# Performance work log

Measured on AMD Instinct MI355X. Metric: run time of the kernel, lower is better.

The kernel has to match this reference:

```python
import jax, jax.numpy as jnp
import numpy as np

EMBED_DIM = 1024
NUM_HEADS = 16
HEAD_DIM = EMBED_DIM // NUM_HEADS
EPS = 1e-5


def setup_inputs() -> dict:
    key = jax.random.key(0)
    ks = jax.random.split(key, 14)
    B, S, E = 2, 2048, EMBED_DIM
    s = 1.0 / np.sqrt(E)
    inp = {
        "x": jax.random.normal(ks[0], (B, S, E), dtype=jnp.float32),
        "Wq": jax.random.normal(ks[1], (E, E), dtype=jnp.float32) * s,
        "bq": jax.random.normal(ks[2], (E,), dtype=jnp.float32) * 0.01,
        "Wk": jax.random.normal(ks[3], (E, E), dtype=jnp.float32) * s,
        "bk": jax.random.normal(ks[4], (E,), dtype=jnp.float32) * 0.01,
        "Wv": jax.random.normal(ks[5], (E, E), dtype=jnp.float32) * s,
        "bv": jax.random.normal(ks[6], (E,), dtype=jnp.float32) * 0.01,
        "Wo": jax.random.normal(ks[7], (E, E), dtype=jnp.float32) * s,
        "bo": jax.random.normal(ks[8], (E,), dtype=jnp.float32) * 0.01,
        "qn_w": jnp.ones((HEAD_DIM,), jnp.float32) + 0.1 * jax.random.normal(ks[9], (HEAD_DIM,), jnp.float32),
        "qn_b": 0.1 * jax.random.normal(ks[10], (HEAD_DIM,), jnp.float32),
        "kn_w": jnp.ones((HEAD_DIM,), jnp.float32) + 0.1 * jax.random.normal(ks[11], (HEAD_DIM,), jnp.float32),
        "kn_b": 0.1 * jax.random.normal(ks[12], (HEAD_DIM,), jnp.float32),
    }
    return inp


def _layernorm(t, w, b):
    # normalize over last axis (head_dim), matching eqx.nn.LayerNorm(eps=1e-5)
    mu = jnp.mean(t, axis=-1, keepdims=True)
    var = jnp.mean(jnp.square(t - mu), axis=-1, keepdims=True)
    return (t - mu) * jax.lax.rsqrt(var + EPS) * w + b


def reference(x, Wq, bq, Wk, bk, Wv, bv, Wo, bo, qn_w, qn_b, kn_w, kn_b):
    B, S, E = x.shape
    H, D = NUM_HEADS, HEAD_DIM
    q = (x @ Wq.T + bq).reshape(B, S, H, D)
    k = (x @ Wk.T + bk).reshape(B, S, H, D)
    v = (x @ Wv.T + bv).reshape(B, S, H, D)
    q = _layernorm(q, qn_w, qn_b)
    k = _layernorm(k, kn_w, kn_b)
    scale = D ** (-0.5)
    # [B,H,S,S] score matrix (faithful to naive implementation)
    scores = jnp.einsum("bqhd,bkhd->bhqk", q, k) * scale
    attn = jax.nn.softmax(scores, axis=-1)
    out = jnp.einsum("bhqk,bkhd->bqhd", attn, v).reshape(B, S, E)
    return out @ Wo.T + bo
```

## Files before the change

kernel.cpp:

```cpp
#include <hip/hip_runtime.h>
#include <stdint.h>


typedef __bf16 bf16_t;
typedef __bf16 bf16x8 __attribute__((ext_vector_type(8)));
typedef __bf16 bf16x4 __attribute__((ext_vector_type(4)));
typedef __bf16 bf16x2 __attribute__((ext_vector_type(2)));
typedef float f32x4 __attribute__((ext_vector_type(4)));
typedef float f32x16 __attribute__((ext_vector_type(16)));
typedef uint32_t u32x4 __attribute__((ext_vector_type(4)));

#define S_LEN 2048
#define QSCALE 0.1803368801f

__device__ __forceinline__ void load_lds16(const void* g, void* l) {
  __builtin_amdgcn_global_load_lds((__attribute__((address_space(1))) void*)g,
                                   (__attribute__((address_space(3))) void*)l,
                                   16, 0, 0);
}

__device__ __forceinline__ f32x4 mfma16(bf16x8 a, bf16x8 b, f32x4 c) {
  return __builtin_amdgcn_mfma_f32_16x16x32_bf16(a, b, c, 0, 0, 0);
}

__device__ __forceinline__ f32x16 mfma32(bf16x8 a, bf16x8 b, f32x16 c) {
  return __builtin_amdgcn_mfma_f32_32x32x16_bf16(a, b, c, 0, 0, 0);
}

__device__ __forceinline__ uint32_t pk_bf16(float a, float b) {
  bf16x2 v; v[0] = (bf16_t)a; v[1] = (bf16_t)b;
  return __builtin_bit_cast(uint32_t, v);
}

__device__ __forceinline__ void plswap(uint32_t& a, uint32_t& b) {
  asm volatile("v_permlane32_swap_b32 %0, %1" : "+v"(a), "+v"(b));
}

__global__ void cvt_all(const float* __restrict__ x, const float* __restrict__ Wq,
                        const float* __restrict__ Wk, const float* __restrict__ Wv,
                        const float* __restrict__ Wo,
                        bf16_t* __restrict__ xb, bf16_t* __restrict__ Wb,
                        bf16_t* __restrict__ Wob) {
  const int bid = blockIdx.x;
  const float* src; bf16_t* dst; int idx;
  if (bid < 4096) { src = x; dst = xb; idx = bid; }
  else {
    const int r = bid - 4096, rg = r >> 10;
    idx = r & 1023;
    if (rg == 0)      { src = Wq; dst = Wb; }
    else if (rg == 1) { src = Wk; dst = Wb + (1 << 20); }
    else if (rg == 2) { src = Wv; dst = Wb + (2 << 20); }
    else              { src = Wo; dst = Wob; }
  }
  const int i = (idx * 256 + threadIdx.x) * 4;
  float4 v = *reinterpret_cast<const float4*>(src + i);
  bf16x4 o;
  o[0] = (bf16_t)v.x; o[1] = (bf16_t)v.y; o[2] = (bf16_t)v.z; o[3] = (bf16_t)v.w;
  *reinterpret_cast<bf16x4*>(dst + i) = o;
}

__launch_bounds__(256, 2)
__global__ void gemm_qkv_ln(const bf16_t* __restrict__ A, const bf16_t* __restrict__ Bt,
                            const float* __restrict__ bq, const float* __restrict__ bk,
                            const float* __restrict__ bv,
                            const float* __restrict__ qnw, const float* __restrict__ qnb,
                            const float* __restrict__ knw, const float* __restrict__ knb,
                            bf16_t* __restrict__ Qb, bf16_t* __restrict__ Kb,
                            bf16_t* __restrict__ Vt) {
  __shared__ alignas(16) bf16_t As[2][128 * 32];
  __shared__ alignas(16) bf16_t Bs[2][128 * 32];
  const int t = threadIdx.x;
  const int orig = blockIdx.y * 24 + blockIdx.x;
  const int logical = (orig & 7) * 96 + (orig >> 3);
  const int bn = logical % 24, bm = logical / 24;
  const int w = t >> 6, lane = t & 63;
  const int wr = w >> 1, wc = w & 1;
  const int lg = lane >> 4, lr = lane & 15;

  f32x4 acc[4][4] = {};
  const int srow = t >> 2;
  const int scol = (t & 3) << 3;
  const bf16_t* ga = A + ((size_t)(bm * 128 + srow) << 10) + scol;
  const bf16_t* gb = Bt + ((size_t)(bn * 128 + srow) << 10) + scol;

#define GSTAGE(buf, k0)                                        \
  {                                                            \
    load_lds16(ga + (k0),         &As[buf][t * 8]);            \
    load_lds16(ga + 65536 + (k0), &As[buf][2048 + t * 8]);     \
    load_lds16(gb + (k0),         &Bs[buf][t * 8]);            \
    load_lds16(gb + 65536 + (k0), &Bs[buf][2048 + t * 8]);     \
  }

  GSTAGE(0, 0);
  __syncthreads();
  for (int it = 0; it < 32; ++it) {
    const int cur = it & 1;
    if (it < 31) GSTAGE(cur ^ 1, (it + 1) << 5);
    bf16x8 af[4], bfr[4];
#pragma unroll
    for (int mt = 0; mt < 4; ++mt)
      af[mt] = *reinterpret_cast<const bf16x8*>(&As[cur][((wr * 64 + mt * 16 + lr) << 5) + lg * 8]);
#pragma unroll
    for (int nt = 0; nt < 4; ++nt)
      bfr[nt] = *reinterpret_cast<const bf16x8*>(&Bs[cur][((wc * 64 + nt * 16 + lr) << 5) + lg * 8]);
#pragma unroll
    for (int mt = 0; mt < 4; ++mt)
#pragma unroll
      for (int nt = 0; nt < 4; ++nt)
        acc[mt][nt] = mfma16(af[mt], bfr[nt], acc[mt][nt]);
    __syncthreads();
  }
#undef GSTAGE

  const int nbase = bn * 128 + wc * 64;
  const int region = nbase >> 10;
  const int h = (nbase & 1023) >> 6;

  if (region == 2) {
#pragma unroll
    for (int mt = 0; mt < 4; ++mt)
#pragma unroll
      for (int r = 0; r < 4; ++r) {
        const int gm = bm * 128 + wr * 64 + mt * 16 + lg * 4 + r;
        const int b = gm >> 11, s = gm & 2047;
#pragma unroll
        for (int nt = 0; nt < 4; ++nt) {
          const int d = nt * 16 + lr;
          float val = acc[mt][nt][r] + bv[h * 64 + d];
          Vt[((size_t)((b * 16 + h) * 64 + d) << 11) + s] = (bf16_t)val;
        }
      }
  } else {
    const float* bias = region ? bk : bq;
    const float* lw = region ? knw : qnw;
    const float* lb = region ? knb : qnb;
    const float osc = region ? 1.0f : QSCALE;
    bf16_t* Outp = region ? Kb : Qb;
#pragma unroll
    for (int mt = 0; mt < 4; ++mt)
#pragma unroll
      for (int r = 0; r < 4; ++r) {
        const int gm = bm * 128 + wr * 64 + mt * 16 + lg * 4 + r;
        const int b = gm >> 11, s = gm & 2047;
        float vv[4], sum = 0.f, sumsq = 0.f;
#pragma unroll
        for (int nt = 0; nt < 4; ++nt) {
          const int d = nt * 16 + lr;
          vv[nt] = acc[mt][nt][r] + bias[h * 64 + d];
          sum += vv[nt];
          sumsq += vv[nt] * vv[nt];
        }
#pragma unroll
        for (int mk = 1; mk < 16; mk <<= 1) {
          sum += __shfl_xor(sum, mk);
          sumsq += __shfl_xor(sumsq, mk);
        }
        const float mean = sum * (1.f / 64.f);
        const float var = sumsq * (1.f / 64.f) - mean * mean;
        const float rstd = rsqrtf(var + 1e-5f);
        const size_t rowoff = ((size_t)((b * 16 + h) * 2048 + s)) << 6;
#pragma unroll
        for (int nt = 0; nt < 4; ++nt) {
          const int d = nt * 16 + lr;
          float y = ((vv[nt] - mean) * rstd * lw[d] + lb[d]) * osc;
          Outp[rowoff + d] = (bf16_t)y;
        }
      }
  }
}

__launch_bounds__(256, 2)
__global__ void gemm_out(const bf16_t* __restrict__ A, const bf16_t* __restrict__ Bt,
                         const float* __restrict__ bo, float* __restrict__ dout) {
  __shared__ alignas(16) bf16_t As[2][64 * 32];
  __shared__ alignas(16) bf16_t Bs[2][128 * 32];
  const int t = threadIdx.x;
  const int orig = blockIdx.y * 8 + blockIdx.x;
  const int logical = (orig & 7) * 64 + (orig >> 3);
  const int bn = logical & 7, bm = logical >> 3;
  const int w = t >> 6, lane = t & 63;
  const int wr = w >> 1, wc = w & 1;
  const int lg = lane >> 4, lr = lane & 15;

  f32x4 acc[2][4] = {};
  const int srow = t >> 2;
  const int scol = (t & 3) << 3;
  const bf16_t* ga = A + ((size_t)(bm * 64 + srow) << 10) + scol;
  const bf16_t* gb = Bt + ((size_t)(bn * 128 + srow) << 10) + scol;

#define OSTAGE(buf, k0)                                        \
  {                                                            \
    load_lds16(ga + (k0),         &As[buf][t * 8]);            \
    load_lds16(gb + (k0),         &Bs[buf][t * 8]);            \
    load_lds16(gb + 65536 + (k0), &Bs[buf][2048 + t * 8]);     \
  }

  OSTAGE(0, 0);
  __syncthreads();
  for (int it = 0; it < 32; ++it) {
    const int cur = it & 1;
    if (it < 31) OSTAGE(cur ^ 1, (it + 1) << 5);
    bf16x8 af[2], bfr[4];
#pragma unroll
    for (int mt = 0; mt < 2; ++mt)
      af[mt] = *reinterpret_cast<const bf16x8*>(&As[cur][((wr * 32 + mt * 16 + lr) << 5) + lg * 8]);
#pragma unroll
    for (int nt = 0; nt < 4; ++nt)
      bfr[nt] = *reinterpret_cast<const bf16x8*>(&Bs[cur][((wc * 64 + nt * 16 + lr) << 5) + lg * 8]);
#pragma unroll
    for (int mt = 0; mt < 2; ++mt)
#pragma unroll
      for (int nt = 0; nt < 4; ++nt)
        acc[mt][nt] = mfma16(af[mt], bfr[nt], acc[mt][nt]);
    __syncthreads();
  }
#undef OSTAGE

#pragma unroll
  for (int mt = 0; mt < 2; ++mt)
#pragma unroll
    for (int r = 0; r < 4; ++r) {
      const int gm = bm * 64 + wr * 32 + mt * 16 + lg * 4 + r;
#pragma unroll
      for (int nt = 0; nt < 4; ++nt) {
        const int gn = bn * 128 + wc * 64 + nt * 16 + lr;
        dout[((size_t)gm << 10) + gn] = acc[mt][nt][r] + bo[gn];
      }
    }
}

template <int NSPLIT>
__launch_bounds__(256, 4)
__global__ void attn_kernel(const bf16_t* __restrict__ Qb, const bf16_t* __restrict__ Kb,
                            const bf16_t* __restrict__ Vt, bf16_t* __restrict__ Og,
                            bf16_t* __restrict__ Op, float* __restrict__ Lp) {
  __shared__ alignas(16) bf16_t KVs[4][64 * 64];

  const int t = threadIdx.x;
  const int w = t >> 6, lane = t & 63;
  const int lq = lane & 31;
  const int hi = lane >> 5;
  const int orig = (blockIdx.z * 32 + blockIdx.y) * 16 + blockIdx.x;
  const int logical = (orig & 7) * (64 * NSPLIT) + (orig >> 3);
  const int qt = logical & 15;
  const int bh = (logical >> 4) & 31;
  const int z = (NSPLIT == 1) ? 0 : (logical >> 9);
  const int b = bh >> 4, h = bh & 15;
  const int q0 = qt * 128 + w * 32;
  const int ntiles = 32 / NSPLIT;

  bf16x8 qf[4];
  {
    const bf16_t* qp = Qb + (((size_t)bh * S_LEN + q0 + lq) << 6) + hi * 8;
#pragma unroll
    for (int c = 0; c < 4; ++c)
      qf[c] = *reinterpret_cast<const bf16x8*>(qp + c * 16);
  }

  f32x16 oacc0 = {}, oacc1 = {}, lacc = {};

  const int krow = (t >> 1) & 63;
  const int kch = ((t >> 7) << 1) | (t & 1);
  const bf16_t* kbase = Kb + (((size_t)bh * S_LEN) << 6) + krow * 64 + kch * 8;
  const bf16_t* vbase = Vt + ((size_t)bh << 17) + krow * S_LEN + kch * 8;

#define STAGE(buf, jt)                                                       \
  {                                                                          \
    const bf16_t* kb_ = kbase + (((size_t)(jt)) << 12);                      \
    const bf16_t* vb_ = vbase + (jt) * 64;                                   \
    load_lds16(kb_,      &KVs[buf][t * 8]);                                  \
    load_lds16(kb_ + 32, &KVs[buf][2048 + t * 8]);                           \
    load_lds16(vb_,      &KVs[2 + (buf)][t * 8]);                            \
    load_lds16(vb_ + 32, &KVs[2 + (buf)][2048 + t * 8]);                     \
  }

  STAGE(0, z * ntiles);
  __syncthreads();

  for (int j = 0; j < ntiles; ++j) {
    const int cur = j & 1;
    if (j < ntiles - 1) STAGE(cur ^ 1, z * ntiles + j + 1);

    f32x16 s0 = {}, s1 = {};
    const bf16_t* kr = &KVs[cur][lq * 16 + hi * 8];
#pragma unroll
    for (int c = 0; c < 4; ++c) {
      bf16x8 kf = *reinterpret_cast<const bf16x8*>(kr + c * 1024);
      s0 = mfma32(kf, qf[c], s0);
    }
#pragma unroll
    for (int c = 0; c < 4; ++c) {
      bf16x8 kf = *reinterpret_cast<const bf16x8*>(kr + 512 + c * 1024);
      s1 = mfma32(kf, qf[c], s1);
    }

    f32x16 p0, p1;
#pragma unroll
    for (int i = 0; i < 16; ++i) p0[i] = __builtin_amdgcn_exp2f(s0[i]);
#pragma unroll
    for (int i = 0; i < 16; ++i) p1[i] = __builtin_amdgcn_exp2f(s1[i]);
    lacc += p0;
    lacc += p1;

    const bf16_t* vr = &KVs[2 + cur][lq * 16 + hi * 8];
#pragma unroll
    for (int c = 0; c < 4; ++c) {
      const f32x16 ph = (c < 2) ? p0 : p1;
      const int cl = c & 1;
      uint32_t w00 = pk_bf16(ph[8 * cl + 0], ph[8 * cl + 1]);
      uint32_t w01 = pk_bf16(ph[8 * cl + 2], ph[8 * cl + 3]);
      uint32_t w10 = pk_bf16(ph[8 * cl + 4], ph[8 * cl + 5]);
      uint32_t w11 = pk_bf16(ph[8 * cl + 6], ph[8 * cl + 7]);
      plswap(w00, w10);
      plswap(w01, w11);
      u32x4 pw = {w00, w01, w10, w11};
      bf16x8 pf = __builtin_bit_cast(bf16x8, pw);
      {
        bf16x8 vf = *reinterpret_cast<const bf16x8*>(vr + c * 1024);
        oacc0 = mfma32(vf, pf, oacc0);
      }
      {
        bf16x8 vf = *reinterpret_cast<const bf16x8*>(vr + 512 + c * 1024);
        oacc1 = mfma32(vf, pf, oacc1);
      }
    }
    __syncthreads();
  }

  float l_;
  {
    float sv[8];
#pragma unroll
    for (int i = 0; i < 8; ++i) sv[i] = lacc[i] + lacc[i + 8];
#pragma unroll
    for (int s2 = 4; s2 >= 1; s2 >>= 1)
#pragma unroll
      for (int i = 0; i < s2; ++i) sv[i] += sv[i + s2];
    l_ = sv[0] + __shfl_xor(sv[0], 32);
  }

  {
    bf16_t* Os = &KVs[0][0] + w * 2048;
    const float inv = (NSPLIT == 1) ? __builtin_amdgcn_rcpf(l_) : 1.0f;
#pragma unroll
    for (int dh = 0; dh < 2; ++dh) {
      const f32x16 oa = dh ? oacc1 : oacc0;
#pragma unroll
      for (int g = 0; g < 8; ++g) {
        const int reg = g * 2;
        const int dl = (reg & 3) + 8 * (reg >> 2) + 4 * hi;
        const int d = dh * 32 + dl;
        const uint32_t wv = pk_bf16(oa[reg] * inv, oa[reg + 1] * inv);
        const int byte = lq * 128 + ((((d >> 3) ^ (lq & 7))) << 4) + ((d & 7) << 1);
        *reinterpret_cast<uint32_t*>(reinterpret_cast<char*>(Os) + byte) = wv;
      }
    }
    if (NSPLIT == 2 && lane < 32)
      Lp[(size_t)(z * 32 + bh) * 2048 + q0 + lq] = l_;
#pragma unroll
    for (int it = 0; it < 4; ++it) {
      const int q = it * 8 + (lane >> 3);
      const int ch = lane & 7;
      bf16x8 ov = *reinterpret_cast<const bf16x8*>(
          reinterpret_cast<char*>(Os) + q * 128 + ((ch ^ (q & 7)) << 4));
      if constexpr (NSPLIT == 1) {
        const size_t gaddr = (((size_t)(b * S_LEN + q0 + q)) << 10) + h * 64 + ch * 8;
        *reinterpret_cast<bf16x8*>(Og + gaddr) = ov;
      } else {
        const size_t rowoff = ((size_t)((z * 32 + bh) * 2048 + q0 + q)) << 6;
        *reinterpret_cast<bf16x8*>(Op + rowoff + ch * 8) = ov;
      }
    }
  }
#undef STAGE
}

__global__ void attn_combine(const bf16_t* __restrict__ Op, const float* __restrict__ Lp,
                             bf16_t* __restrict__ Ob) {
  const int gid = blockIdx.x * 256 + threadIdx.x;
  const int row = gid >> 3, ch = gid & 7;
  const bf16_t* o1 = Op + ((size_t)row << 6) + ch * 8;
  const bf16_t* o2 = o1 + (1u << 22);
  const float inv = 1.f / (Lp[row] + Lp[(1u << 16) + row]);
  bf16x8 v1 = *reinterpret_cast<const bf16x8*>(o1);
  bf16x8 v2 = *reinterpret_cast<const bf16x8*>(o2);
  bf16x8 o;
#pragma unroll
  for (int i = 0; i < 8; ++i) o[i] = (bf16_t)(((float)v1[i] + (float)v2[i]) * inv);
  const int bh = row >> 11, s = row & 2047;
  const int b = bh >> 4, h = bh & 15;
  *reinterpret_cast<bf16x8*>(Ob + (((size_t)(b * S_LEN + s)) << 10) + h * 64 + ch * 8) = o;
}

extern "C" void kernel_launch(void* const* d_in, const int* in_sizes, int n_in,
                              void* d_out, int out_size, void* d_ws, size_t ws_size,
                              hipStream_t stream) {
  const float* x = (const float*)d_in[0];
  const float* Wq = (const float*)d_in[1];
  const float* bq = (const float*)d_in[2];
  const float* Wk = (const float*)d_in[3];
  const float* bk = (const float*)d_in[4];
  const float* Wv = (const float*)d_in[5];
  const float* bv = (const float*)d_in[6];
  const float* Wo = (const float*)d_in[7];
  const float* bo = (const float*)d_in[8];
  const float* qnw = (const float*)d_in[9];
  const float* qnb = (const float*)d_in[10];
  const float* knw = (const float*)d_in[11];
  const float* knb = (const float*)d_in[12];
  float* out = (float*)d_out;

  uint8_t* ws = (uint8_t*)d_ws;
  bf16_t* xb = (bf16_t*)(ws + 0);
  bf16_t* Wb = (bf16_t*)(ws + 8388608);
  bf16_t* Wob = (bf16_t*)(ws + 14680064);
  bf16_t* Qb = (bf16_t*)(ws + 16777216);
  bf16_t* Kb = (bf16_t*)(ws + 25165824);
  bf16_t* Vt = (bf16_t*)(ws + 33554432);
  bf16_t* Ob = (bf16_t*)(ws + 41943040);
  bf16_t* Opart = (bf16_t*)(ws + 50331648);
  float*  Lpart = (float*)(ws + 67108864);
  const bool split = ws_size >= 67633152ull;

  cvt_all<<<8192, 256, 0, stream>>>(x, Wq, Wk, Wv, Wo, xb, Wb, Wob);

  gemm_qkv_ln<<<dim3(24, 32), 256, 0, stream>>>(xb, Wb, bq, bk, bv, qnw, qnb, knw, knb,
                                                Qb, Kb, Vt);
  if (split) {
    attn_kernel<2><<<dim3(16, 32, 2), 256, 0, stream>>>(Qb, Kb, Vt, Ob, Opart, Lpart);
    attn_combine<<<2048, 256, 0, stream>>>(Opart, Lpart, Ob);
  } else {
    attn_kernel<1><<<dim3(16, 32, 1), 256, 0, stream>>>(Qb, Kb, Vt, Ob, Opart, Lpart);
  }
  gemm_out<<<dim3(8, 64), 256, 0, stream>>>(Ob, Wob, bo, out);
}
```

Measured before the change: 117.7 us.

## Fuse split-attention combine into output projection GEMM A-operand staging

Removes the separate attn_combine kernel. In split mode the output GEMM now loads both partial attention outputs and their softmax denominators directly from global memory into registers, combines and normalizes them, and writes bf16 to LDS as the A tile. This saves a kernel launch and the write and re-read of the combined Ob buffer. In exchange, each of the 8 column blocks redundantly reads and combines the same partial rows, and A staging now goes through registers instead of async global-to-LDS loads.

```diff
diff --git a/kernel.cpp b/kernel.cpp
--- a/kernel.cpp
+++ b/kernel.cpp
@@ -169,9 +169,11 @@
   }
 }
 
+template <bool SPLIT>
 __launch_bounds__(256, 2)
 __global__ void gemm_out(const bf16_t* __restrict__ A, const bf16_t* __restrict__ Bt,
-                         const float* __restrict__ bo, float* __restrict__ dout) {
+                         const float* __restrict__ bo, float* __restrict__ dout,
+                         const bf16_t* __restrict__ Op, const float* __restrict__ Lp) {
   __shared__ alignas(16) bf16_t As[2][64 * 32];
   __shared__ alignas(16) bf16_t Bs[2][128 * 32];
   const int t = threadIdx.x;
@@ -187,19 +189,52 @@
   const int scol = (t & 3) << 3;
   const bf16_t* ga = A + ((size_t)(bm * 64 + srow) << 10) + scol;
   const bf16_t* gb = Bt + ((size_t)(bn * 128 + srow) << 10) + scol;
-
-#define OSTAGE(buf, k0)                                        \
+  const int bA = (bm * 64) >> 11;
+  const int sA = ((bm * 64) & 2047) + srow;
+
+  bf16x8 v1n, v2n; float l1n, l2n;
+
+#define LOADA(k0)                                                            \
+  {                                                                          \
+    const int e_ = (k0) + scol;                                              \
+    const int h_ = e_ >> 6, d_ = e_ & 63;                                    \
+    const size_t pr_ = (size_t)(bA * 16 + h_) * 2048 + sA;                   \
+    v1n = *reinterpret_cast<const bf16x8*>(Op + (pr_ << 6) + d_);            \
+    v2n = *reinterpret_cast<const bf16x8*>(Op + ((pr_ + 65536) << 6) + d_);  \
+    l1n = Lp[pr_]; l2n = Lp[pr_ + 65536];                                    \
+  }
+#define WRITEA(buf)                                                          \
+  {                                                                          \
+    const float inv_ = __builtin_amdgcn_rcpf(l1n + l2n);                     \
+    u32x4 aw_;                                                               \
+    _Pragma("unroll")                                                        \
+    for (int i_ = 0; i_ < 4; ++i_)                                           \
+      aw_[i_] = pk_bf16(((float)v1n[2 * i_] + (float)v2n[2 * i_]) * inv_,    \
+                        ((float)v1n[2 * i_ + 1] + (float)v2n[2 * i_ + 1]) * inv_); \
+    *reinterpret_cast<u32x4*>(&As[buf][t * 8]) = aw_;                        \
+  }
+#define STAGEB(buf, k0)                                        \
   {                                                            \
-    load_lds16(ga + (k0),         &As[buf][t * 8]);            \
     load_lds16(gb + (k0),         &Bs[buf][t * 8]);            \
     load_lds16(gb + 65536 + (k0), &Bs[buf][2048 + t * 8]);     \
   }
 
-  OSTAGE(0, 0);
+  if constexpr (SPLIT) {
+    LOADA(0);
+    STAGEB(0, 0);
+    WRITEA(0);
+  } else {
+    load_lds16(ga, &As[0][t * 8]);
+    STAGEB(0, 0);
+  }
   __syncthreads();
   for (int it = 0; it < 32; ++it) {
     const int cur = it & 1;
-    if (it < 31) OSTAGE(cur ^ 1, (it + 1) << 5);
+    if (it < 31) {
+      if constexpr (SPLIT) { LOADA((it + 1) << 5); }
+      else                 { load_lds16(ga + ((it + 1) << 5), &As[cur ^ 1][t * 8]); }
+      STAGEB(cur ^ 1, (it + 1) << 5);
+    }
     bf16x8 af[2], bfr[4];
 #pragma unroll
     for (int mt = 0; mt < 2; ++mt)
@@ -212,9 +247,12 @@
 #pragma unroll
       for (int nt = 0; nt < 4; ++nt)
         acc[mt][nt] = mfma16(af[mt], bfr[nt], acc[mt][nt]);
+    if (SPLIT && it < 31) WRITEA(cur ^ 1);
     __syncthreads();
   }
-#undef OSTAGE
+#undef LOADA
+#undef WRITEA
+#undef STAGEB
 
 #pragma unroll
   for (int mt = 0; mt < 2; ++mt)
@@ -373,23 +411,6 @@
     }
   }
 #undef STAGE
-}
-
-__global__ void attn_combine(const bf16_t* __restrict__ Op, const float* __restrict__ Lp,
-                             bf16_t* __restrict__ Ob) {
-  const int gid = blockIdx.x * 256 + threadIdx.x;
-  const int row = gid >> 3, ch = gid & 7;
-  const bf16_t* o1 = Op + ((size_t)row << 6) + ch * 8;
-  const bf16_t* o2 = o1 + (1u << 22);
-  const float inv = 1.f / (Lp[row] + Lp[(1u << 16) + row]);
-  bf16x8 v1 = *reinterpret_cast<const bf16x8*>(o1);
-  bf16x8 v2 = *reinterpret_cast<const bf16x8*>(o2);
-  bf16x8 o;
-#pragma unroll
-  for (int i = 0; i < 8; ++i) o[i] = (bf16_t)(((float)v1[i] + (float)v2[i]) * inv);
-  const int bh = row >> 11, s = row & 2047;
-  const int b = bh >> 4, h = bh & 15;
-  *reinterpret_cast<bf16x8*>(Ob + (((size_t)(b * S_LEN + s)) << 10) + h * 64 + ch * 8) = o;
 }
 
 extern "C" void kernel_launch(void* const* d_in, const int* in_sizes, int n_in,
@@ -428,9 +449,9 @@
                                                 Qb, Kb, Vt);
   if (split) {
     attn_kernel<2><<<dim3(16, 32, 2), 256, 0, stream>>>(Qb, Kb, Vt, Ob, Opart, Lpart);
-    attn_combine<<<2048, 256, 0, stream>>>(Opart, Lpart, Ob);
+    gemm_out<true><<<dim3(8, 64), 256, 0, stream>>>(Ob, Wob, bo, out, Opart, Lpart);
   } else {
     attn_kernel<1><<<dim3(16, 32, 1), 256, 0, stream>>>(Qb, Kb, Vt, Ob, Opart, Lpart);
-  }
-  gemm_out<<<dim3(8, 64), 256, 0, stream>>>(Ob, Wob, bo, out);
-}
+    gemm_out<false><<<dim3(8, 64), 256, 0, stream>>>(Ob, Wob, bo, out, Opart, Lpart);
+  }
+}
```

Result: slower. 122.4 us (+4.0%).
